# Performance work log

Hardware: AMD Instinct MI355X
Metric: run time of the kernel (lower is better)

The kernel has to match this reference:

```python
import jax, jax.numpy as jnp
import numpy as np

HIDDEN = 1024
HEADS = 16
HEAD_DIM = HIDDEN // HEADS


def setup_inputs() -> dict:
    key = jax.random.key(0)
    ks = jax.random.split(key, 9)
    B, S = 2, 2048
    std = 1.0 / np.sqrt(HIDDEN)
    inp = {
        'hidden_states': jax.random.normal(ks[0], (B, S, HIDDEN), dtype=jnp.float32),
        'attention_mask': jnp.ones((B, S), dtype=jnp.int32),
        'wq': jax.random.normal(ks[1], (HIDDEN, HIDDEN), dtype=jnp.float32) * std,
        'bq': jnp.zeros((HIDDEN,), dtype=jnp.float32),
        'wk': jax.random.normal(ks[2], (HIDDEN, HIDDEN), dtype=jnp.float32) * std,
        'bk': jnp.zeros((HIDDEN,), dtype=jnp.float32),
        'wv': jax.random.normal(ks[3], (HIDDEN, HIDDEN), dtype=jnp.float32) * std,
        'bv': jnp.zeros((HIDDEN,), dtype=jnp.float32),
        'wo': jax.random.normal(ks[4], (HIDDEN, HIDDEN), dtype=jnp.float32) * std,
        'bo': jnp.zeros((HIDDEN,), dtype=jnp.float32),
    }
    return inp


def reference(hidden_states, attention_mask, wq, bq, wk, bk, wv, bv, wo, bo):
    B, S, H = hidden_states.shape
    def heads(x):  # [B,S,H] -> [B,nh,S,hd]
        return x.reshape(B, S, HEADS, HEAD_DIM).transpose(0, 2, 1, 3)
    q = heads(hidden_states @ wq + bq)
    k = heads(hidden_states @ wk + bk)
    v = heads(hidden_states @ wv + bv)
    scores = jnp.einsum('bhqd,bhkd->bhqk', q, k) / np.sqrt(HEAD_DIM).astype(np.float32)
    causal = jnp.tril(jnp.ones((S, S), dtype=bool))  # True = keep
    keep = causal[None, None] & (attention_mask[:, None, None, :] != 0)
    scores = jnp.where(keep, scores, -jnp.inf)
    probs = jax.nn.softmax(scores, axis=-1)
    out = jnp.einsum('bhqk,bhkd->bhqd', probs, v)  # [B,nh,S,hd]
    out = out.transpose(0, 2, 1, 3).reshape(B, S, H)
    return out @ wo + bo
```

## Files before the change

kernel.cpp:

```cpp
#include <hip/hip_runtime.h>

#define HID   1024
#define SLEN  2048
#define NHEAD 16
#define HDIM  64
#define SC2L  0.18033688f

typedef unsigned short u16;
typedef _Float16 f16;
using bf16x8 = __attribute__((ext_vector_type(8))) short;
using h16x2  = __attribute__((ext_vector_type(2))) __fp16;
using f16x4  = __attribute__((ext_vector_type(4))) f16;
using f32x4  = __attribute__((ext_vector_type(4))) float;

typedef __attribute__((address_space(1))) void gvoid;
typedef __attribute__((address_space(3))) void lvoid;

__device__ __forceinline__ u16 f2bf(float f) {
  union { float f; unsigned u; } v; v.f = f;
  unsigned u = v.u;
  return (u16)((u + 0x7fffu + ((u >> 16) & 1u)) >> 16);
}

__device__ __forceinline__ void async_ld16(const u16* g, u16* l) {
  __builtin_amdgcn_global_load_lds((gvoid*)g, (lvoid*)l, 16, 0, 0);
}

__global__ __launch_bounds__(256) void prep_kernel(const float* __restrict__ x,
                                                   const float* __restrict__ wq,
                                                   const float* __restrict__ wk,
                                                   const float* __restrict__ wv,
                                                   const float* __restrict__ wo,
                                                   u16* __restrict__ xb,
                                                   u16* __restrict__ wt) {
  const int tid = threadIdx.x;
  if (blockIdx.z == 4) {
    const int bid = blockIdx.y * 32 + blockIdx.x;
#pragma unroll
    for (int it = 0; it < 4; ++it) {
      const int i = bid * 1024 + it * 256 + tid;
      float4 v = ((const float4*)x)[i];
      ushort4 o;
      o.x = f2bf(v.x); o.y = f2bf(v.y); o.z = f2bf(v.z); o.w = f2bf(v.w);
      ((ushort4*)xb)[i] = o;
    }
    return;
  }
  const float* src = (blockIdx.z == 0) ? wq : (blockIdx.z == 1) ? wk
                   : (blockIdx.z == 2) ? wv : wo;
  u16* dst = wt + (size_t)blockIdx.z * (HID * HID);
  __shared__ float tile[32][33];
  const int n0 = blockIdx.x * 32, k0 = blockIdx.y * 32;
  const int xx = tid & 31, yy = tid >> 5;
  for (int i = yy; i < 32; i += 8)
    tile[i][xx] = src[(size_t)(k0 + i) * HID + n0 + xx];
  __syncthreads();
  for (int i = yy; i < 32; i += 8)
    dst[(size_t)(n0 + i) * HID + k0 + xx] = f2bf(tile[xx][i]);
}

__global__ __launch_bounds__(256) void gemm_qkv_kernel(const u16* __restrict__ A,
                                                       const u16* __restrict__ Bt,
                                                       const float* __restrict__ bq,
                                                       const float* __restrict__ bk,
                                                       const float* __restrict__ bv,
                                                       u16* __restrict__ Qb,
                                                       u16* __restrict__ Kb,
                                                       u16* __restrict__ VTf) {
  __shared__ u16 smem[8192];
  u16* sA = smem;
  u16* sB = smem + 4096;
  const int tid  = threadIdx.x;
  const int wave = tid >> 6, lane = tid & 63;
  const int quad = lane >> 4, l16 = lane & 15;
  const int n0g = blockIdx.x * 128;
  const int region = blockIdx.x >> 3;
  const int colbase = (blockIdx.x & 7) * 128;
  const int m0 = blockIdx.y * 128;
  const int wm = (wave & 1) * 64, wn = (wave >> 1) * 64;

  f32x4 acc[4][4] = {};
  const int srow = lane >> 2;
  const int scol = (lane & 3) * 8;

  for (int kt = 0; kt < HID; kt += 32) {
    __syncthreads();
    for (int c = wave; c < 8; c += 4) {
      async_ld16(A  + (size_t)(m0  + c * 16 + srow) * HID + kt + scol, &sA[c * 512]);
      async_ld16(Bt + (size_t)(n0g + c * 16 + srow) * HID + kt + scol, &sB[c * 512]);
    }
    __syncthreads();

    bf16x8 af[4], bfr[4];
#pragma unroll
    for (int t = 0; t < 4; ++t) {
      af[t]  = *(const bf16x8*)&sA[(wm + t * 16 + l16) * 32 + quad * 8];
      bfr[t] = *(const bf16x8*)&sB[(wn + t * 16 + l16) * 32 + quad * 8];
    }
#pragma unroll
    for (int mt = 0; mt < 4; ++mt)
#pragma unroll
      for (int nt = 0; nt < 4; ++nt)
        acc[mt][nt] = __builtin_amdgcn_mfma_f32_16x16x32_bf16(af[mt], bfr[nt],
                                                              acc[mt][nt], 0, 0, 0);
  }

  const float* bias = (region == 0) ? bq : (region == 1) ? bk : bv;
  float bvv[4];
#pragma unroll
  for (int nt = 0; nt < 4; ++nt) bvv[nt] = bias[colbase + wn + nt * 16 + l16];

  if (region == 2) {
    const int bb = m0 >> 11;
    const int m0loc = m0 & 2047;
    const int h0 = colbase >> 6;
    u16* T = smem;
#pragma unroll
    for (int h2 = 0; h2 < 2; ++h2) {
      __syncthreads();
      if ((wave >> 1) == h2) {
#pragma unroll
        for (int mt = 0; mt < 4; ++mt)
#pragma unroll
          for (int nt = 0; nt < 4; ++nt)
#pragma unroll
            for (int r = 0; r < 4; ++r) {
              const int sl = (wave & 1) * 64 + mt * 16 + quad * 4 + r;
              const int dl = nt * 16 + l16;
              union { f16 h; u16 u; } cv;
              cv.h = (f16)(acc[mt][nt][r] + bvv[nt]);
              T[dl * 128 + (((sl >> 3) ^ l16) * 8) + (sl & 7)] = cv.u;
            }
      }
      __syncthreads();
      const int d = tid >> 2, sg = (tid & 3) * 4;
      u16* slab0 = VTf + ((size_t)((bb * NHEAD + h0 + h2) * 128 + (m0loc >> 4))) * 1024;
#pragma unroll
      for (int cc = 0; cc < 4; ++cc) {
        const int cl = sg + cc;
        const int ph = cl ^ (d & 15);
        const int slot = (d * 2 + (cl & 1)) ^ ((d >> 2) & 1);
        *(bf16x8*)(slab0 + (size_t)(cl >> 1) * 1024 + slot * 8)
            = *(const bf16x8*)&T[d * 128 + ph * 8];
      }
    }
    return;
  }

  u16* C = (region == 0) ? Qb : Kb;
#pragma unroll
  for (int mt = 0; mt < 4; ++mt)
#pragma unroll
    for (int r = 0; r < 4; ++r) {
      const int row = m0 + wm + mt * 16 + quad * 4 + r;
#pragma unroll
      for (int nt = 0; nt < 4; ++nt) {
        const int col = colbase + wn + nt * 16 + l16;
        C[(size_t)row * HID + col] = f2bf(acc[mt][nt][r] + bvv[nt]);
      }
    }
}

__global__ __launch_bounds__(256) void gemm_o_kernel(const u16* __restrict__ A,
                                                     const u16* __restrict__ Bt,
                                                     const float* __restrict__ bias,
                                                     float* __restrict__ Cf) {
  __shared__ u16 sA[64 * 32];
  __shared__ u16 sB[128 * 32];
  const int tid  = threadIdx.x;
  const int wave = tid >> 6, lane = tid & 63;
  const int quad = lane >> 4, l16 = lane & 15;
  const int n0 = blockIdx.x * 128;
  const int m0 = blockIdx.y * 64;
  const int wn = wave * 32;

  f32x4 acc[4][2] = {};
  const int srow = lane >> 2;
  const int scol = (lane & 3) * 8;

  for (int kt = 0; kt < HID; kt += 32) {
    __syncthreads();
    for (int c = wave; c < 12; c += 4) {
      if (c < 4) async_ld16(A  + (size_t)(m0 + c * 16 + srow) * HID + kt + scol, &sA[c * 512]);
      else       async_ld16(Bt + (size_t)(n0 + (c - 4) * 16 + srow) * HID + kt + scol,
                            &sB[(c - 4) * 512]);
    }
    __syncthreads();

    bf16x8 af[4], bfr[2];
#pragma unroll
    for (int t = 0; t < 4; ++t)
      af[t] = *(const bf16x8*)&sA[(t * 16 + l16) * 32 + quad * 8];
#pragma unroll
    for (int t = 0; t < 2; ++t)
      bfr[t] = *(const bf16x8*)&sB[(wn + t * 16 + l16) * 32 + quad * 8];
#pragma unroll
    for (int mt = 0; mt < 4; ++mt)
#pragma unroll
      for (int nt = 0; nt < 2; ++nt)
        acc[mt][nt] = __builtin_amdgcn_mfma_f32_16x16x32_bf16(af[mt], bfr[nt],
                                                              acc[mt][nt], 0, 0, 0);
  }

  float bvv[2];
#pragma unroll
  for (int nt = 0; nt < 2; ++nt) bvv[nt] = bias[n0 + wn + nt * 16 + l16];
#pragma unroll
  for (int mt = 0; mt < 4; ++mt)
#pragma unroll
    for (int r = 0; r < 4; ++r) {
      const int row = m0 + mt * 16 + quad * 4 + r;
#pragma unroll
      for (int nt = 0; nt < 2; ++nt)
        Cf[(size_t)row * HID + n0 + wn + nt * 16 + l16] = acc[mt][nt][r] + bvv[nt];
    }
}

__global__ __launch_bounds__(256, 2) void flash_attn_kernel(const u16* __restrict__ Q,
                                                            const u16* __restrict__ K,
                                                            const u16* __restrict__ VT,
                                                            const int* __restrict__ mask,
                                                            u16* __restrict__ O) {
  const int qt = 31 - blockIdx.x;
  const int h = blockIdx.y, b = blockIdx.z;
  const int tid  = threadIdx.x;
  const int wave = tid >> 6, lane = tid & 63;
  const int quad = lane >> 4, l16 = lane & 15;

  __shared__ alignas(16) char smraw[35840];
  u16*   Ks  = (u16*)smraw;
  u16*   Vt  = (u16*)(smraw + 16384);
  float* Ob0 = (float*)smraw;
  float* Ob1 = (float*)(smraw + 16896);
  float* lb  = (float*)(smraw + 33792);

  const u16* Kh  = K  + (size_t)b * SLEN * HID + h * HDIM;
  const u16* Vth = VT + (size_t)(b * NHEAD + h) * (128 * 1024);

  const int srow8 = lane >> 3;
  const int gch   = (lane & 7) ^ srow8;
  const int rx    = l16 & 7;

  unsigned mw = 0;
  {
    const int4* mrow = (const int4*)(mask + b * SLEN);
#pragma unroll
    for (int c = 0; c < 8; ++c) {
      int4 m = mrow[lane * 8 + c];
      mw |= (m.x ? 1u : 0u) << (c * 4);
      mw |= (m.y ? 1u : 0u) << (c * 4 + 1);
      mw |= (m.z ? 1u : 0u) << (c * 4 + 2);
      mw |= (m.w ? 1u : 0u) << (c * 4 + 3);
    }
  }
  const int mb = (wave & 1) * 16 + quad * 4;

  const int q0 = qt * 64;

  bf16x8 qb[4][2];
#pragma unroll
  for (int nt = 0; nt < 4; ++nt) {
    const u16* qp = Q + (size_t)(b * SLEN + q0 + nt * 16 + l16) * HID + h * HDIM + quad * 8;
    qb[nt][0] = *(const bf16x8*)qp;
    qb[nt][1] = *(const bf16x8*)(qp + 32);
  }

  f32x4 oacc[4][4] = {};
  float l_part[4] = {0.f, 0.f, 0.f, 0.f};

  const int r0s = wave * 16 + srow8;
#define STAGE_KV(jt, bufi)                                                      \
  {                                                                             \
    u16* kd = Ks + (bufi) * 4096 + wave * 1024;                                 \
    async_ld16(Kh + (size_t)((jt) * 64 + r0s) * HID + gch * 8,       kd);       \
    async_ld16(Kh + (size_t)((jt) * 64 + r0s + 8) * HID + gch * 8,   kd + 512); \
    const u16* vs = Vth + (size_t)((jt) * 4 + wave) * 1024;                     \
    u16* vd = Vt + (bufi) * 4096 + wave * 1024;                                 \
    async_ld16(vs + lane * 8,        vd);                                       \
    async_ld16(vs + (64 + lane) * 8, vd + 512);                                 \
  }

  STAGE_KV(0, 0);

  for (int j = 0; j <= qt; ++j) {
    const int buf = j & 1;
    u16* KsB = Ks + buf * 4096;
    u16* VtB = Vt + buf * 4096;

    if (j < qt) {
      STAGE_KV(j + 1, buf ^ 1);
      asm volatile("s_waitcnt vmcnt(6)" ::: "memory");
    } else {
      asm volatile("s_waitcnt vmcnt(2)" ::: "memory");
    }

    const unsigned wbits = __shfl(mw, 2 * j + (wave >> 1));
    float map[4];
#pragma unroll
    for (int r = 0; r < 4; ++r)
      map[r] = ((wbits >> (mb + r)) & 1u) ? 0.f : -1e30f;

    const u16* kp = KsB + (wave * 16 + l16) * 64;
    const int ph0 = quad ^ rx;
    const bf16x8 ka0 = *(const bf16x8*)(kp + ph0 * 8);
    const bf16x8 ka1 = *(const bf16x8*)(kp + (ph0 ^ 4) * 8);

    float p[4][4];
    __builtin_amdgcn_s_setprio(1);
#pragma unroll
    for (int nt = 0; nt < 4; ++nt) {
      f32x4 z = {0.f, 0.f, 0.f, 0.f};
      z = __builtin_amdgcn_mfma_f32_16x16x32_bf16(ka0, qb[nt][0], z, 0, 0, 0);
      z = __builtin_amdgcn_mfma_f32_16x16x32_bf16(ka1, qb[nt][1], z, 0, 0, 0);
#pragma unroll
      for (int r = 0; r < 4; ++r)
        p[nt][r] = exp2f(fmaf(z[r], SC2L, map[r]));
    }
    __builtin_amdgcn_s_setprio(0);
    if (j == qt) {
#pragma unroll
      for (int nt = 0; nt < 4; ++nt)
#pragma unroll
        for (int r = 0; r < 4; ++r)
          if (wave * 16 + quad * 4 + r > nt * 16 + l16) p[nt][r] = 0.f;
    }

    f16x4 pb[4];
#pragma unroll
    for (int nt = 0; nt < 4; ++nt) {
      l_part[nt] += (p[nt][0] + p[nt][1]) + (p[nt][2] + p[nt][3]);
      union { h16x2 h[2]; f16x4 v; } u;
      u.h[0] = __builtin_amdgcn_cvt_pkrtz(p[nt][0], p[nt][1]);
      u.h[1] = __builtin_amdgcn_cvt_pkrtz(p[nt][2], p[nt][3]);
      pb[nt] = u.v;
    }

    if (j < qt) {
      asm volatile("s_waitcnt vmcnt(4)" ::: "memory");
    } else {
      asm volatile("s_waitcnt vmcnt(0)" ::: "memory");
    }

    __builtin_amdgcn_s_setprio(1);
#pragma unroll
    for (int dt = 0; dt < 4; ++dt) {
      const int dd = dt * 16 + l16;
      const int slot = (dd * 2 + (quad >> 1)) ^ ((dd >> 2) & 1);
      const f16x4 va = *(const f16x4*)(VtB + wave * 1024 + slot * 8 + (quad & 1) * 4);
#pragma unroll
      for (int nt = 0; nt < 4; ++nt)
        oacc[dt][nt] = __builtin_amdgcn_mfma_f32_16x16x16f16(va, pb[nt], oacc[dt][nt], 0, 0, 0);
    }
    __builtin_amdgcn_s_setprio(0);
  }
#undef STAGE_KV

  __syncthreads();

#pragma unroll
  for (int nt = 0; nt < 4; ++nt) {
    l_part[nt] += __shfl_xor(l_part[nt], 16);
    l_part[nt] += __shfl_xor(l_part[nt], 32);
  }
  if (quad == 0)
#pragma unroll
    for (int nt = 0; nt < 4; ++nt) lb[wave * 64 + nt * 16 + l16] = l_part[nt];

  if ((wave & 1) == 0) {
    float* ob = (wave == 0) ? Ob0 : Ob1;
#pragma unroll
    for (int dt = 0; dt < 4; ++dt)
#pragma unroll
      for (int nt = 0; nt < 4; ++nt)
#pragma unroll
        for (int r = 0; r < 4; ++r)
          ob[(dt * 16 + quad * 4 + r) * 66 + nt * 16 + l16] = oacc[dt][nt][r];
  }
  __syncthreads();
  if (wave & 1) {
    float* ob = (wave == 1) ? Ob0 : Ob1;
#pragma unroll
    for (int dt = 0; dt < 4; ++dt)
#pragma unroll
      for (int nt = 0; nt < 4; ++nt)
#pragma unroll
        for (int r = 0; r < 4; ++r)
          ob[(dt * 16 + quad * 4 + r) * 66 + nt * 16 + l16] += oacc[dt][nt][r];
  }
  __syncthreads();

  {
    const int q  = tid >> 2;
    const int dc = tid & 3;
    const float l = lb[q] + lb[64 + q] + lb[128 + q] + lb[192 + q];
    const float inv = 1.f / l;
    u16 ob[16];
#pragma unroll
    for (int e = 0; e < 16; ++e) {
      const int d = dc * 16 + e;
      ob[e] = f2bf((Ob0[d * 66 + q] + Ob1[d * 66 + q]) * inv);
    }
    u16* op = O + (size_t)(b * SLEN + q0 + q) * HID + h * HDIM + dc * 16;
    *(bf16x8*)op       = *(bf16x8*)&ob[0];
    *(bf16x8*)(op + 8) = *(bf16x8*)&ob[8];
  }
}

extern "C" void kernel_launch(void* const* d_in, const int* in_sizes, int n_in,
                              void* d_out, int out_size, void* d_ws, size_t ws_size,
                              hipStream_t stream) {
  const float* x    = (const float*)d_in[0];
  const int*   mask = (const int*)d_in[1];
  const float* wq   = (const float*)d_in[2];
  const float* bq   = (const float*)d_in[3];
  const float* wk   = (const float*)d_in[4];
  const float* bk   = (const float*)d_in[5];
  const float* wv   = (const float*)d_in[6];
  const float* bv   = (const float*)d_in[7];
  const float* wo   = (const float*)d_in[8];
  const float* bo   = (const float*)d_in[9];
  float* out = (float*)d_out;

  char* ws = (char*)d_ws;
  u16* XBF = (u16*)(ws);
  u16* WT  = (u16*)(ws + (8u  << 20));
  u16* QBF = (u16*)(ws + (16u << 20));
  u16* KBF = (u16*)(ws + (24u << 20));
  u16* VTF = (u16*)(ws + (32u << 20));
  u16* ATT = (u16*)(ws);

  prep_kernel<<<dim3(32, 32, 5), 256, 0, stream>>>(x, wq, wk, wv, wo, XBF, WT);
  gemm_qkv_kernel<<<dim3(24, 32), 256, 0, stream>>>(XBF, WT, bq, bk, bv, QBF, KBF, VTF);
  flash_attn_kernel<<<dim3(32, NHEAD, 2), 256, 0, stream>>>(QBF, KBF, VTF, mask, ATT);
  gemm_o_kernel<<<dim3(8, 64), 256, 0, stream>>>(ATT, WT + (3u << 20), bo, out);
}
```

Before: 220.4 us.

## Double-buffer GEMM K-loop loads and pair causal query tiles per attention block

Both projection GEMMs now prefetch the next K-slice into a second LDS buffer while computing the current one, using vmcnt waits and barriers in place of two syncthreads per step. The flash attention kernel now has each block process two query tiles, xb and 31-xb, so every block does the same amount of causal work, and the grid is halved. This is meant to hide global load latency and remove the tail imbalance from triangular work. In exchange it doubles GEMM shared memory and halves attention grid parallelism (512 blocks).

```diff
diff --git a/kernel.cpp b/kernel.cpp
--- a/kernel.cpp
+++ b/kernel.cpp
@@ -67,9 +67,7 @@
                                                        u16* __restrict__ Qb,
                                                        u16* __restrict__ Kb,
                                                        u16* __restrict__ VTf) {
-  __shared__ u16 smem[8192];
-  u16* sA = smem;
-  u16* sB = smem + 4096;
+  __shared__ u16 smem[16384];
   const int tid  = threadIdx.x;
   const int wave = tid >> 6, lane = tid & 63;
   const int quad = lane >> 4, l16 = lane & 15;
@@ -83,14 +81,27 @@
   const int srow = lane >> 2;
   const int scol = (lane & 3) * 8;
 
-  for (int kt = 0; kt < HID; kt += 32) {
-    __syncthreads();
-    for (int c = wave; c < 8; c += 4) {
-      async_ld16(A  + (size_t)(m0  + c * 16 + srow) * HID + kt + scol, &sA[c * 512]);
-      async_ld16(Bt + (size_t)(n0g + c * 16 + srow) * HID + kt + scol, &sB[c * 512]);
-    }
-    __syncthreads();
-
+#define STAGE_G(kt, bi)                                                          \
+  for (int c = wave; c < 8; c += 4) {                                            \
+    async_ld16(A  + (size_t)(m0  + c * 16 + srow) * HID + (kt) + scol,           \
+               &smem[(bi) * 8192 + c * 512]);                                    \
+    async_ld16(Bt + (size_t)(n0g + c * 16 + srow) * HID + (kt) + scol,           \
+               &smem[(bi) * 8192 + 4096 + c * 512]);                             \
+  }
+
+  STAGE_G(0, 0);
+  for (int ks = 0; ks < 32; ++ks) {
+    const int bi = ks & 1;
+    if (ks < 31) {
+      STAGE_G((ks + 1) * 32, bi ^ 1);
+      asm volatile("s_waitcnt vmcnt(4)" ::: "memory");
+    } else {
+      asm volatile("s_waitcnt vmcnt(0)" ::: "memory");
+    }
+    __builtin_amdgcn_s_barrier();
+
+    const u16* sA = smem + bi * 8192;
+    const u16* sB = smem + bi * 8192 + 4096;
     bf16x8 af[4], bfr[4];
 #pragma unroll
     for (int t = 0; t < 4; ++t) {
@@ -103,7 +114,9 @@
       for (int nt = 0; nt < 4; ++nt)
         acc[mt][nt] = __builtin_amdgcn_mfma_f32_16x16x32_bf16(af[mt], bfr[nt],
                                                               acc[mt][nt], 0, 0, 0);
-  }
+    __builtin_amdgcn_s_barrier();
+  }
+#undef STAGE_G
 
   const float* bias = (region == 0) ? bq : (region == 1) ? bk : bv;
   float bvv[4];
@@ -165,8 +178,7 @@
                                                      const u16* __restrict__ Bt,
                                                      const float* __restrict__ bias,
                                                      float* __restrict__ Cf) {
-  __shared__ u16 sA[64 * 32];
-  __shared__ u16 sB[128 * 32];
+  __shared__ u16 smem[12288];
   const int tid  = threadIdx.x;
   const int wave = tid >> 6, lane = tid & 63;
   const int quad = lane >> 4, l16 = lane & 15;
@@ -178,15 +190,27 @@
   const int srow = lane >> 2;
   const int scol = (lane & 3) * 8;
 
-  for (int kt = 0; kt < HID; kt += 32) {
-    __syncthreads();
-    for (int c = wave; c < 12; c += 4) {
-      if (c < 4) async_ld16(A  + (size_t)(m0 + c * 16 + srow) * HID + kt + scol, &sA[c * 512]);
-      else       async_ld16(Bt + (size_t)(n0 + (c - 4) * 16 + srow) * HID + kt + scol,
-                            &sB[(c - 4) * 512]);
-    }
-    __syncthreads();
-
+#define STAGE_O(kt, bi)                                                          \
+  for (int c = wave; c < 12; c += 4) {                                           \
+    if (c < 4) async_ld16(A + (size_t)(m0 + c * 16 + srow) * HID + (kt) + scol,  \
+                          &smem[(bi) * 6144 + c * 512]);                         \
+    else async_ld16(Bt + (size_t)(n0 + (c - 4) * 16 + srow) * HID + (kt) + scol, \
+                    &smem[(bi) * 6144 + 2048 + (c - 4) * 512]);                  \
+  }
+
+  STAGE_O(0, 0);
+  for (int ks = 0; ks < 32; ++ks) {
+    const int bi = ks & 1;
+    if (ks < 31) {
+      STAGE_O((ks + 1) * 32, bi ^ 1);
+      asm volatile("s_waitcnt vmcnt(3)" ::: "memory");
+    } else {
+      asm volatile("s_waitcnt vmcnt(0)" ::: "memory");
+    }
+    __builtin_amdgcn_s_barrier();
+
+    const u16* sA = smem + bi * 6144;
+    const u16* sB = smem + bi * 6144 + 2048;
     bf16x8 af[4], bfr[2];
 #pragma unroll
     for (int t = 0; t < 4; ++t)
@@ -200,7 +224,9 @@
       for (int nt = 0; nt < 2; ++nt)
         acc[mt][nt] = __builtin_amdgcn_mfma_f32_16x16x32_bf16(af[mt], bfr[nt],
                                                               acc[mt][nt], 0, 0, 0);
-  }
+    __builtin_amdgcn_s_barrier();
+  }
+#undef STAGE_O
 
   float bvv[2];
 #pragma unroll
@@ -221,8 +247,7 @@
                                                             const u16* __restrict__ VT,
                                                             const int* __restrict__ mask,
                                                             u16* __restrict__ O) {
-  const int qt = 31 - blockIdx.x;
-  const int h = blockIdx.y, b = blockIdx.z;
+  const int xb = blockIdx.x, h = blockIdx.y, b = blockIdx.z;
   const int tid  = threadIdx.x;
   const int wave = tid >> 6, lane = tid & 63;
   const int quad = lane >> 4, l16 = lane & 15;
@@ -254,19 +279,6 @@
     }
   }
   const int mb = (wave & 1) * 16 + quad * 4;
-
-  const int q0 = qt * 64;
-
-  bf16x8 qb[4][2];
-#pragma unroll
-  for (int nt = 0; nt < 4; ++nt) {
-    const u16* qp = Q + (size_t)(b * SLEN + q0 + nt * 16 + l16) * HID + h * HDIM + quad * 8;
-    qb[nt][0] = *(const bf16x8*)qp;
-    qb[nt][1] = *(const bf16x8*)(qp + 32);
-  }
-
-  f32x4 oacc[4][4] = {};
-  float l_part[4] = {0.f, 0.f, 0.f, 0.f};
 
   const int r0s = wave * 16 + srow8;
 #define STAGE_KV(jt, bufi)                                                      \
@@ -280,130 +292,147 @@
     async_ld16(vs + (64 + lane) * 8, vd + 512);                                 \
   }
 
-  STAGE_KV(0, 0);
-
-  for (int j = 0; j <= qt; ++j) {
-    const int buf = j & 1;
-    u16* KsB = Ks + buf * 4096;
-    u16* VtB = Vt + buf * 4096;
-
-    if (j < qt) {
-      STAGE_KV(j + 1, buf ^ 1);
-      asm volatile("s_waitcnt vmcnt(6)" ::: "memory");
-    } else {
-      asm volatile("s_waitcnt vmcnt(2)" ::: "memory");
-    }
-
-    const unsigned wbits = __shfl(mw, 2 * j + (wave >> 1));
-    float map[4];
-#pragma unroll
-    for (int r = 0; r < 4; ++r)
-      map[r] = ((wbits >> (mb + r)) & 1u) ? 0.f : -1e30f;
-
-    const u16* kp = KsB + (wave * 16 + l16) * 64;
-    const int ph0 = quad ^ rx;
-    const bf16x8 ka0 = *(const bf16x8*)(kp + ph0 * 8);
-    const bf16x8 ka1 = *(const bf16x8*)(kp + (ph0 ^ 4) * 8);
-
-    float p[4][4];
-    __builtin_amdgcn_s_setprio(1);
+  for (int phase = 0; phase < 2; ++phase) {
+    const int qt = phase ? (31 - xb) : xb;
+    const int q0 = qt * 64;
+
+    bf16x8 qb[4][2];
 #pragma unroll
     for (int nt = 0; nt < 4; ++nt) {
-      f32x4 z = {0.f, 0.f, 0.f, 0.f};
-      z = __builtin_amdgcn_mfma_f32_16x16x32_bf16(ka0, qb[nt][0], z, 0, 0, 0);
-      z = __builtin_amdgcn_mfma_f32_16x16x32_bf16(ka1, qb[nt][1], z, 0, 0, 0);
+      const u16* qp = Q + (size_t)(b * SLEN + q0 + nt * 16 + l16) * HID + h * HDIM + quad * 8;
+      qb[nt][0] = *(const bf16x8*)qp;
+      qb[nt][1] = *(const bf16x8*)(qp + 32);
+    }
+
+    f32x4 oacc[4][4] = {};
+    float l_part[4] = {0.f, 0.f, 0.f, 0.f};
+
+    STAGE_KV(0, 0);
+
+    for (int j = 0; j <= qt; ++j) {
+      const int buf = j & 1;
+      u16* KsB = Ks + buf * 4096;
+      u16* VtB = Vt + buf * 4096;
+
+      if (j < qt) {
+        STAGE_KV(j + 1, buf ^ 1);
+        asm volatile("s_waitcnt vmcnt(6)" ::: "memory");
+      } else {
+        asm volatile("s_waitcnt vmcnt(2)" ::: "memory");
+      }
+
+      const unsigned wbits = __shfl(mw, 2 * j + (wave >> 1));
+      float map[4];
 #pragma unroll
       for (int r = 0; r < 4; ++r)
-        p[nt][r] = exp2f(fmaf(z[r], SC2L, map[r]));
-    }
-    __builtin_amdgcn_s_setprio(0);
-    if (j == qt) {
-#pragma unroll
-      for (int nt = 0; nt < 4; ++nt)
+        map[r] = ((wbits >> (mb + r)) & 1u) ? 0.f : -1e30f;
+
+      const u16* kp = KsB + (wave * 16 + l16) * 64;
+      const int ph0 = quad ^ rx;
+      const bf16x8 ka0 = *(const bf16x8*)(kp + ph0 * 8);
+      const bf16x8 ka1 = *(const bf16x8*)(kp + (ph0 ^ 4) * 8);
+
+      float p[4][4];
+      __builtin_amdgcn_s_setprio(1);
+#pragma unroll
+      for (int nt = 0; nt < 4; ++nt) {
+        f32x4 z = {0.f, 0.f, 0.f, 0.f};
+        z = __builtin_amdgcn_mfma_f32_16x16x32_bf16(ka0, qb[nt][0], z, 0, 0, 0);
+        z = __builtin_amdgcn_mfma_f32_16x16x32_bf16(ka1, qb[nt][1], z, 0, 0, 0);
 #pragma unroll
         for (int r = 0; r < 4; ++r)
-          if (wave * 16 + quad * 4 + r > nt * 16 + l16) p[nt][r] = 0.f;
-    }
-
-    f16x4 pb[4];
+          p[nt][r] = exp2f(fmaf(z[r], SC2L, map[r]));
+      }
+      __builtin_amdgcn_s_setprio(0);
+      if (j == qt) {
+#pragma unroll
+        for (int nt = 0; nt < 4; ++nt)
+#pragma unroll
+          for (int r = 0; r < 4; ++r)
+            if (wave * 16 + quad * 4 + r > nt * 16 + l16) p[nt][r] = 0.f;
+      }
+
+      f16x4 pb[4];
+#pragma unroll
+      for (int nt = 0; nt < 4; ++nt) {
+        l_part[nt] += (p[nt][0] + p[nt][1]) + (p[nt][2] + p[nt][3]);
+        union { h16x2 h[2]; f16x4 v; } u;
+        u.h[0] = __builtin_amdgcn_cvt_pkrtz(p[nt][0], p[nt][1]);
+        u.h[1] = __builtin_amdgcn_cvt_pkrtz(p[nt][2], p[nt][3]);
+        pb[nt] = u.v;
+      }
+
+      if (j < qt) {
+        asm volatile("s_waitcnt vmcnt(4)" ::: "memory");
+      } else {
+        asm volatile("s_waitcnt vmcnt(0)" ::: "memory");
+      }
+
+      __builtin_amdgcn_s_setprio(1);
+#pragma unroll
+      for (int dt = 0; dt < 4; ++dt) {
+        const int dd = dt * 16 + l16;
+        const int slot = (dd * 2 + (quad >> 1)) ^ ((dd >> 2) & 1);
+        const f16x4 va = *(const f16x4*)(VtB + wave * 1024 + slot * 8 + (quad & 1) * 4);
+#pragma unroll
+        for (int nt = 0; nt < 4; ++nt)
+          oacc[dt][nt] = __builtin_amdgcn_mfma_f32_16x16x16f16(va, pb[nt], oacc[dt][nt], 0, 0, 0);
+      }
+      __builtin_amdgcn_s_setprio(0);
+    }
+
+    __syncthreads();
+
 #pragma unroll
     for (int nt = 0; nt < 4; ++nt) {
-      l_part[nt] += (p[nt][0] + p[nt][1]) + (p[nt][2] + p[nt][3]);
-      union { h16x2 h[2]; f16x4 v; } u;
-      u.h[0] = __builtin_amdgcn_cvt_pkrtz(p[nt][0], p[nt][1]);
-      u.h[1] = __builtin_amdgcn_cvt_pkrtz(p[nt][2], p[nt][3]);
-      pb[nt] = u.v;
-    }
-
-    if (j < qt) {
-      asm volatile("s_waitcnt vmcnt(4)" ::: "memory");
-    } else {
-      asm volatile("s_waitcnt vmcnt(0)" ::: "memory");
-    }
-
-    __builtin_amdgcn_s_setprio(1);
-#pragma unroll
-    for (int dt = 0; dt < 4; ++dt) {
-      const int dd = dt * 16 + l16;
-      const int slot = (dd * 2 + (quad >> 1)) ^ ((dd >> 2) & 1);
-      const f16x4 va = *(const f16x4*)(VtB + wave * 1024 + slot * 8 + (quad & 1) * 4);
-#pragma unroll
-      for (int nt = 0; nt < 4; ++nt)
-        oacc[dt][nt] = __builtin_amdgcn_mfma_f32_16x16x16f16(va, pb[nt], oacc[dt][nt], 0, 0, 0);
-    }
-    __builtin_amdgcn_s_setprio(0);
+      l_part[nt] += __shfl_xor(l_part[nt], 16);
+      l_part[nt] += __shfl_xor(l_part[nt], 32);
+    }
+    if (quad == 0)
+#pragma unroll
+      for (int nt = 0; nt < 4; ++nt) lb[wave * 64 + nt * 16 + l16] = l_part[nt];
+
+    if ((wave & 1) == 0) {
+      float* ob = (wave == 0) ? Ob0 : Ob1;
+#pragma unroll
+      for (int dt = 0; dt < 4; ++dt)
+#pragma unroll
+        for (int nt = 0; nt < 4; ++nt)
+#pragma unroll
+          for (int r = 0; r < 4; ++r)
+            ob[(dt * 16 + quad * 4 + r) * 66 + nt * 16 + l16] = oacc[dt][nt][r];
+    }
+    __syncthreads();
+    if (wave & 1) {
+      float* ob = (wave == 1) ? Ob0 : Ob1;
+#pragma unroll
+      for (int dt = 0; dt < 4; ++dt)
+#pragma unroll
+        for (int nt = 0; nt < 4; ++nt)
+#pragma unroll
+          for (int r = 0; r < 4; ++r)
+            ob[(dt * 16 + quad * 4 + r) * 66 + nt * 16 + l16] += oacc[dt][nt][r];
+    }
+    __syncthreads();
+
+    {
+      const int q  = tid >> 2;
+      const int dc = tid & 3;
+      const float l = lb[q] + lb[64 + q] + lb[128 + q] + lb[192 + q];
+      const float inv = 1.f / l;
+      u16 ob[16];
+#pragma unroll
+      for (int e = 0; e < 16; ++e) {
+        const int d = dc * 16 + e;
+        ob[e] = f2bf((Ob0[d * 66 + q] + Ob1[d * 66 + q]) * inv);
+      }
+      u16* op = O + (size_t)(b * SLEN + q0 + q) * HID + h * HDIM + dc * 16;
+      *(bf16x8*)op       = *(bf16x8*)&ob[0];
+      *(bf16x8*)(op + 8) = *(bf16x8*)&ob[8];
+    }
+    __syncthreads();
   }
 #undef STAGE_KV
-
-  __syncthreads();
-
-#pragma unroll
-  for (int nt = 0; nt < 4; ++nt) {
-    l_part[nt] += __shfl_xor(l_part[nt], 16);
-    l_part[nt] += __shfl_xor(l_part[nt], 32);
-  }
-  if (quad == 0)
-#pragma unroll
-    for (int nt = 0; nt < 4; ++nt) lb[wave * 64 + nt * 16 + l16] = l_part[nt];
-
-  if ((wave & 1) == 0) {
-    float* ob = (wave == 0) ? Ob0 : Ob1;
-#pragma unroll
-    for (int dt = 0; dt < 4; ++dt)
-#pragma unroll
-      for (int nt = 0; nt < 4; ++nt)
-#pragma unroll
-        for (int r = 0; r < 4; ++r)
-          ob[(dt * 16 + quad * 4 + r) * 66 + nt * 16 + l16] = oacc[dt][nt][r];
-  }
-  __syncthreads();
-  if (wave & 1) {
-    float* ob = (wave == 1) ? Ob0 : Ob1;
-#pragma unroll
-    for (int dt = 0; dt < 4; ++dt)
-#pragma unroll
-      for (int nt = 0; nt < 4; ++nt)
-#pragma unroll
-        for (int r = 0; r < 4; ++r)
-          ob[(dt * 16 + quad * 4 + r) * 66 + nt * 16 + l16] += oacc[dt][nt][r];
-  }
-  __syncthreads();
-
-  {
-    const int q  = tid >> 2;
-    const int dc = tid & 3;
-    const float l = lb[q] + lb[64 + q] + lb[128 + q] + lb[192 + q];
-    const float inv = 1.f / l;
-    u16 ob[16];
-#pragma unroll
-    for (int e = 0; e < 16; ++e) {
-      const int d = dc * 16 + e;
-      ob[e] = f2bf((Ob0[d * 66 + q] + Ob1[d * 66 + q]) * inv);
-    }
-    u16* op = O + (size_t)(b * SLEN + q0 + q) * HID + h * HDIM + dc * 16;
-    *(bf16x8*)op       = *(bf16x8*)&ob[0];
-    *(bf16x8*)(op + 8) = *(bf16x8*)&ob[8];
-  }
 }
 
 extern "C" void kernel_launch(void* const* d_in, const int* in_sizes, int n_in,
@@ -431,6 +460,6 @@
 
   prep_kernel<<<dim3(32, 32, 5), 256, 0, stream>>>(x, wq, wk, wv, wo, XBF, WT);
   gemm_qkv_kernel<<<dim3(24, 32), 256, 0, stream>>>(XBF, WT, bq, bk, bv, QBF, KBF, VTF);
-  flash_attn_kernel<<<dim3(32, NHEAD, 2), 256, 0, stream>>>(QBF, KBF, VTF, mask, ATT);
+  flash_attn_kernel<<<dim3(16, NHEAD, 2), 256, 0, stream>>>(QBF, KBF, VTF, mask, ATT);
   gemm_o_kernel<<<dim3(8, 64), 256, 0, stream>>>(ATT, WT + (3u << 20), bo, out);
 }
```

After: 198.3 us. 1.11x faster.
